# Optimization experiments

Measured on AMD Instinct MI355X. Metric: run time of the kernel, lower is better.

Reference implementation:

```python
import jax, jax.numpy as jnp
import numpy as np

S = 3      # num_scales
CIN = 3    # in_channels (hardcoded by expand(...,3,...) in source)
COUT = 3   # out_channels (forced by final broadcast)
K = 3
PAD = 1


def setup_inputs() -> dict:
    key = jax.random.key(0)
    ks = jax.random.split(key, 8)
    B, H, W = 4, 384, 384
    x = jax.random.normal(ks[0], (B, CIN, H, W), jnp.float32)
    # params follow the torch inits: theta,sigma ~ U(0,pi); f0,theta0 = 1
    theta = jax.random.uniform(ks[1], (S, COUT, CIN), jnp.float32) * jnp.pi
    sigma = jax.random.uniform(ks[2], (S, COUT, CIN), jnp.float32) * jnp.pi
    f0 = jnp.ones((S, COUT, CIN), jnp.float32)
    theta0 = jnp.ones((S, COUT, CIN), jnp.float32)
    attn_w1 = jax.random.normal(ks[3], (64, CIN), jnp.float32) * 0.1     # 1x1 conv weight
    attn_b1 = jnp.zeros((64,), jnp.float32)
    attn_w2 = jax.random.normal(ks[4], (COUT * S, 64), jnp.float32) * 0.1
    attn_b2 = jnp.zeros((COUT * S,), jnp.float32)
    conv_w = jax.random.normal(ks[5], (COUT, CIN, K, K), jnp.float32) * 0.05
    mixing = jax.random.uniform(ks[6], (1,), jnp.float32)
    band = jax.random.uniform(ks[7], (COUT, CIN, 2), jnp.float32)        # freq_band_select ~ U(0,1)
    return dict(x=x, theta=theta, sigma=sigma, f0=f0, theta0=theta0,
                attn_w1=attn_w1, attn_b1=attn_b1, attn_w2=attn_w2, attn_b2=attn_b2,
                conv_w=conv_w, mixing=mixing, band=band)


def _log_gabor_bank(theta, sigma, f0, theta0, H, W):
    # vectorized over all scales: returns [S, Co, Cin, H, W] real filter bank
    yy, xx = jnp.meshgrid(jnp.linspace(-1.0, 1.0, H), jnp.linspace(-1.0, 1.0, W), indexing='ij')
    r = jnp.sqrt(xx * xx + yy * yy + 1e-6)          # [H,W]
    phi = jnp.arctan2(yy, xx)                        # [H,W]
    f0e = f0[..., None, None]                        # [S,Co,Cin,1,1]
    sig = sigma[..., None, None]
    th = theta[..., None, None]
    th0 = theta0[..., None, None]
    log_gabor = jnp.exp(-jnp.log(r - jnp.log(f0e)) ** 2 / (2.0 * jnp.log(sig) ** 2))
    angular = jnp.exp(-(phi - th) ** 2 / (2.0 * th0 ** 2))
    return log_gabor * angular


def _forward(x, theta, sigma, f0, theta0, attn_w1, attn_b1, attn_w2, attn_b2, conv_w, mixing, band):
    B, Cin, H, W = x.shape
    # torch.fft.fftshift with no dim shifts ALL axes (incl. batch/channel) -- replicate exactly
    x_freq_shift = jnp.fft.fftshift(jnp.fft.fft2(x))                 # [B,Cin,H,W] complex64

    filt = _log_gabor_bank(theta, sigma, f0, theta0, H, W)           # [S,Co,Cin,H,W]

    # attention net: 1x1 conv -> relu -> 1x1 conv -> softmax over channel dim
    mag = jnp.abs(x_freq_shift)
    h1 = jax.nn.relu(jnp.einsum('bchw,oc->bohw', mag, attn_w1) + attn_b1[None, :, None, None])
    logits = jnp.einsum('bchw,oc->bohw', h1, attn_w2) + attn_b2[None, :, None, None]
    attn = jax.nn.softmax(logits, axis=1).reshape(B, S, COUT, H, W)

    # attended[b,d,h,w] = sum_{s,co} attn[b,s,co,h,w] * xfreq[b,d,h,w] * filt[s,co,d,h,w]
    wgt = jnp.einsum('bschw,scdhw->bdhw', attn, filt)                # real [B,Cin,H,W]
    attended = (x_freq_shift * wgt).sum(axis=1)                      # [B,H,W] complex

    # per-(out,in)-channel square band mask, indices from height (as in source)
    start_idx = jnp.floor((band[..., 0] + 1.0) / 2.0 * H).astype(jnp.int32)   # [Co,Cin]
    end_idx = jnp.floor((band[..., 1] + 1.0) / 2.0 * H).astype(jnp.int32)
    ih = jnp.arange(H)
    rm = (ih[None, None, :] >= start_idx[..., None]) & (ih[None, None, :] < end_idx[..., None])
    iw = jnp.arange(W)
    cm = (iw[None, None, :] >= start_idx[..., None]) & (iw[None, None, :] < end_idx[..., None])
    mask = (rm[..., :, None] & cm[..., None, :]).astype(x.dtype)     # [Co,Cin,H,W]

    # broadcast quirk in source: [B,1,H,W] * [B,Co,1,Cin,H,W] -> [B,Co,B,Cin,H,W]
    six = mask[None, :, None, :, :, :] * attended[None, None, :, None, :, :]
    six = jnp.broadcast_to(six, (B, COUT, B, Cin, H, W))
    # torch ifftshift with no dim shifts ALL 6 axes; ifft2 transforms last two
    x_filtered = jnp.fft.ifft2(jnp.fft.ifftshift(six)).real          # [B,Co,B,Cin,H,W]

    x_spatial = jax.lax.conv_general_dilated(
        x, conv_w, window_strides=(1, 1), padding=[(PAD, PAD), (PAD, PAD)],
        dimension_numbers=('NCHW', 'OIHW', 'NCHW'))                  # [B,Co,H,W]

    mix = mixing[0]
    return mix * x_filtered + (1.0 - mix) * x_spatial[None, None]    # [B,Co,B,Cin,H,W]


def reference(x, theta, sigma, f0, theta0, attn_w1, attn_b1, attn_w2, attn_b2, conv_w, mixing, band):
    return _forward(x, theta, sigma, f0, theta0, attn_w1, attn_b1, attn_w2, attn_b2, conv_w, mixing, band)
```

## Files before the change

### kernel.cpp

```cpp
#include <hip/hip_runtime.h>
#include <math.h>

#define N384 384
#define NPIX 147456
#define LSTRIDE 385
#define LINES 8

__device__ __forceinline__ float2 cmul(float2 a, float2 b) {
    return make_float2(a.x*b.x - a.y*b.y, a.x*b.y + a.y*b.x);
}

__device__ __forceinline__ void build_tw(float2* tw, int tid) {
    for (int k = tid; k < 384; k += 256) {
        float sn, cs;
        sincospif((float)k * (2.0f / 384.0f), &sn, &cs);
        tw[k] = make_float2(cs, sn);
    }
}

template <int SGNI>
__device__ float2* fft384x8(float2* b0, float2* b1, const float2* tw, int tid) {
    float2* src = b0;
    float2* dst = b1;
    const int line = tid >> 5;
    const int l32  = tid & 31;
    const float SG = (float)SGNI;
    const float s3 = SG * 0.86602540378443864676f;

    {
        float2* L = src + line * LSTRIDE;
        float2* D = dst + line * LSTRIDE;
#pragma unroll
        for (int q = 0; q < 2; ++q) {
            int i = l32 + 32 * q;
            float2 e0 = L[i],       e1 = L[i + 128], e2 = L[i + 256];
            float2 o0 = L[i + 64],  o1 = L[i + 192], o2 = L[i + 320];
            float t1x = e1.x + e2.x, t1y = e1.y + e2.y;
            float t2x = e1.x - e2.x, t2y = e1.y - e2.y;
            float2 E0 = make_float2(e0.x + t1x, e0.y + t1y);
            float mx = e0.x - 0.5f * t1x, my = e0.y - 0.5f * t1y;
            float ux = -s3 * t2y, uy = s3 * t2x;
            float2 E1 = make_float2(mx + ux, my + uy);
            float2 E2 = make_float2(mx - ux, my - uy);
            float s1x = o1.x + o2.x, s1y = o1.y + o2.y;
            float s2x = o1.x - o2.x, s2y = o1.y - o2.y;
            float2 O0 = make_float2(o0.x + s1x, o0.y + s1y);
            float nx = o0.x - 0.5f * s1x, ny = o0.y - 0.5f * s1y;
            float vx = -s3 * s2y, vy = s3 * s2x;
            float2 O1 = make_float2(nx + vx, ny + vy);
            float2 O2 = make_float2(nx - vx, ny - vy);
            float2 T1 = make_float2(0.5f * O1.x - s3 * O1.y, 0.5f * O1.y + s3 * O1.x);
            float2 T2 = make_float2(-0.5f * O2.x - s3 * O2.y, -0.5f * O2.y + s3 * O2.x);
            float2 y0 = make_float2(E0.x + O0.x, E0.y + O0.y);
            float2 y3 = make_float2(E0.x - O0.x, E0.y - O0.y);
            float2 y1 = make_float2(E1.x + T1.x, E1.y + T1.y);
            float2 y4 = make_float2(E1.x - T1.x, E1.y - T1.y);
            float2 y2 = make_float2(E2.x + T2.x, E2.y + T2.y);
            float2 y5 = make_float2(E2.x - T2.x, E2.y - T2.y);
            float2 c1 = tw[i], c2 = tw[2 * i], c3 = tw[3 * i], c4 = tw[4 * i], c5 = tw[5 * i];
            int o = 6 * i;
            D[o]     = y0;
            D[o + 1] = cmul(y1, make_float2(c1.x, SG * c1.y));
            D[o + 2] = cmul(y2, make_float2(c2.x, SG * c2.y));
            D[o + 3] = cmul(y3, make_float2(c3.x, SG * c3.y));
            D[o + 4] = cmul(y4, make_float2(c4.x, SG * c4.y));
            D[o + 5] = cmul(y5, make_float2(c5.x, SG * c5.y));
        }
    }
    __syncthreads();
    { float2* t = src; src = dst; dst = t; }

#pragma unroll
    for (int st = 0; st < 2; ++st) {
        const int s = (st == 0) ? 6 : 24;
        float2* L = src + line * LSTRIDE;
        float2* D = dst + line * LSTRIDE;
#pragma unroll
        for (int q = 0; q < 3; ++q) {
            int i = l32 + 32 * q;
            int k = i % s;
            int js = i - k;
            float2 A0 = L[i];
            float2 A1 = L[i + 96];
            float2 A2 = L[i + 192];
            float2 A3 = L[i + 288];
            float t0x = A0.x + A2.x, t0y = A0.y + A2.y;
            float t1x = A0.x - A2.x, t1y = A0.y - A2.y;
            float t2x = A1.x + A3.x, t2y = A1.y + A3.y;
            float t3x = A1.x - A3.x, t3y = A1.y - A3.y;
            float u3x = -SG * t3y,   u3y = SG * t3x;
            float2 y0 = make_float2(t0x + t2x, t0y + t2y);
            float2 y2 = make_float2(t0x - t2x, t0y - t2y);
            float2 y1 = make_float2(t1x + u3x, t1y + u3y);
            float2 y3 = make_float2(t1x - u3x, t1y - u3y);
            float2 c1 = tw[js], c2 = tw[2 * js], c3 = tw[3 * js];
            float2 w1 = make_float2(c1.x, SG * c1.y);
            float2 w2 = make_float2(c2.x, SG * c2.y);
            float2 w3 = make_float2(c3.x, SG * c3.y);
            int o = i + 3 * js;
            D[o]         = y0;
            D[o + s]     = cmul(y1, w1);
            D[o + 2 * s] = cmul(y2, w2);
            D[o + 3 * s] = cmul(y3, w3);
        }
        __syncthreads();
        { float2* t = src; src = dst; dst = t; }
    }

    {
        float2* L = src + line * LSTRIDE;
        float2* D = dst + line * LSTRIDE;
#pragma unroll
        for (int q = 0; q < 3; ++q) {
            int i = l32 + 32 * q;
            float2 A0 = L[i];
            float2 A1 = L[i + 96];
            float2 A2 = L[i + 192];
            float2 A3 = L[i + 288];
            float t0x = A0.x + A2.x, t0y = A0.y + A2.y;
            float t1x = A0.x - A2.x, t1y = A0.y - A2.y;
            float t2x = A1.x + A3.x, t2y = A1.y + A3.y;
            float t3x = A1.x - A3.x, t3y = A1.y - A3.y;
            float u3x = -SG * t3y,   u3y = SG * t3x;
            D[i]       = make_float2(t0x + t2x, t0y + t2y);
            D[i + 96]  = make_float2(t1x + u3x, t1y + u3y);
            D[i + 192] = make_float2(t0x - t2x, t0y - t2y);
            D[i + 288] = make_float2(t1x - u3x, t1y - u3y);
        }
    }
    __syncthreads();
    return dst;
}

__global__ __launch_bounds__(256) void k_fwd_rows(const float* __restrict__ x,
                                                  float2* __restrict__ F1) {
    __shared__ float2 sbuf[2][LINES * LSTRIDE];
    __shared__ float2 tw[384];
    int img = blockIdx.y;
    int rg  = blockIdx.x;
    int tid = threadIdx.x;
    build_tw(tw, tid);
    const float4* xim = (const float4*)(x + (size_t)img * NPIX + (size_t)rg * 16 * 384);
    for (int idx4 = tid; idx4 < 1536; idx4 += 256) {
        int row = idx4 / 96;
        int e   = (idx4 - row * 96) * 4;
        float4 v = xim[idx4];
        float* L = (float*)(sbuf[0] + (row >> 1) * LSTRIDE + e) + (row & 1);
        L[0] = v.x; L[2] = v.y; L[4] = v.z; L[6] = v.w;
    }
    __syncthreads();
    float2* res = fft384x8<-1>(sbuf[0], sbuf[1], tw, tid);
    float2* F1b = F1 + (size_t)img * NPIX + (size_t)rg * 16 * 384;
    for (int it = tid; it < 1536; it += 256) {
        int line = it / 192;
        int k2   = it - line * 192;
        const float2* L = res + line * LSTRIDE;
        float2 A = L[k2];
        int m = (k2 == 0) ? 0 : 384 - k2;
        float2 B = L[m];
        float2 X1 = make_float2(0.5f * (A.x + B.x), 0.5f * (A.y - B.y));
        float2 X2 = make_float2(0.5f * (A.y + B.y), 0.5f * (B.x - A.x));
        F1b[(size_t)(2 * line) * 384 + k2]     = X1;
        F1b[(size_t)(2 * line + 1) * 384 + k2] = X2;
    }
}

__global__ __launch_bounds__(256) void k_fwd_cols(const float2* __restrict__ In,
                                                  float2* __restrict__ Out) {
    __shared__ float2 sbuf[2][LINES * LSTRIDE];
    __shared__ float2 tw[384];
    int img = blockIdx.y;
    int cg  = blockIdx.x;
    int tid = threadIdx.x;
    build_tw(tw, tid);
    const float4* inim = (const float4*)(In + (size_t)img * NPIX + cg * 8);
    int c = tid & 3, hb = tid >> 2;
    for (int q = 0; q < 6; ++q) {
        int h = hb + 64 * q;
        float4 v = inim[(size_t)h * 192 + c];
        sbuf[0][(2 * c) * LSTRIDE + h]     = make_float2(v.x, v.y);
        sbuf[0][(2 * c + 1) * LSTRIDE + h] = make_float2(v.z, v.w);
    }
    __syncthreads();
    float2* res = fft384x8<-1>(sbuf[0], sbuf[1], tw, tid);
    float4* outim = (float4*)(Out + (size_t)img * NPIX + cg * 8);
    for (int q = 0; q < 3; ++q) {
        int h = hb + 64 * q;
        float2 a = res[(2 * c) * LSTRIDE + h];
        float2 b = res[(2 * c + 1) * LSTRIDE + h];
        outim[(size_t)h * 192 + c] = make_float4(a.x, a.y, b.x, b.y);
    }
}

__global__ __launch_bounds__(192) void k_attn(const float2* __restrict__ F2,
                                              const float* __restrict__ theta,
                                              const float* __restrict__ sigma,
                                              const float* __restrict__ f0,
                                              const float* __restrict__ theta0,
                                              const float* __restrict__ aw1,
                                              const float* __restrict__ ab1,
                                              const float* __restrict__ aw2,
                                              const float* __restrict__ ab2,
                                              const float* __restrict__ band,
                                              float2* __restrict__ A) {
    __shared__ float4 par[27];
    int tid = threadIdx.x;
    if (tid < 27) {
        float lf0 = logf(f0[tid]);
        float ls  = logf(sigma[tid]);
        float na  = -0.5f / (ls * ls);
        float th  = theta[tid];
        float t0  = theta0[tid];
        float nb  = -0.5f / (t0 * t0);
        par[tid] = make_float4(lf0, na, th, nb);
    }
    __syncthreads();

    int h = 192 + blockIdx.x;
    int w = 192 + tid;

    bool needed = false;
#pragma unroll
    for (int q = 0; q < 9; ++q) {
        int s = (int)floorf((band[2 * q + 0] + 1.0f) * 0.5f * 384.0f);
        int e = (int)floorf((band[2 * q + 1] + 1.0f) * 0.5f * 384.0f);
        needed |= (h >= s) && (h < e) && (w >= s) && (w < e);
    }
    if (__ballot(needed) == 0ULL) return;

    int hs = h - 192;
    int ws = w - 192;

    float2 xf[4][3];
    float  mag[4][3];
#pragma unroll
    for (int b = 0; b < 4; ++b) {
        int bp = (b + 2) & 3;
#pragma unroll
        for (int c = 0; c < 3; ++c) {
            int cp = c + 2; if (cp >= 3) cp -= 3;
            float2 v = F2[(size_t)(bp * 3 + cp) * NPIX + (size_t)hs * 384 + ws];
            xf[b][c]  = v;
            mag[b][c] = sqrtf(v.x * v.x + v.y * v.y);
        }
    }

    float lgt[4][9];
#pragma unroll
    for (int b = 0; b < 4; ++b)
#pragma unroll
        for (int j = 0; j < 9; ++j) lgt[b][j] = ab2[j];
    for (int o = 0; o < 64; ++o) {
        float w0 = aw1[o * 3 + 0], w1 = aw1[o * 3 + 1], w2 = aw1[o * 3 + 2];
        float bb = ab1[o];
        float hv[4];
#pragma unroll
        for (int b = 0; b < 4; ++b)
            hv[b] = fmaxf(bb + w0 * mag[b][0] + w1 * mag[b][1] + w2 * mag[b][2], 0.0f);
#pragma unroll
        for (int j = 0; j < 9; ++j) {
            float wj = aw2[j * 64 + o];
#pragma unroll
            for (int b = 0; b < 4; ++b) lgt[b][j] += wj * hv[b];
        }
    }

    float yy = -1.0f + 2.0f * (float)h / 383.0f;
    float xx = -1.0f + 2.0f * (float)w / 383.0f;
    float r   = sqrtf(xx * xx + yy * yy + 1e-6f);
    float phi = atan2f(yy, xx);
    float filt[27];
#pragma unroll
    for (int i = 0; i < 27; ++i) {
        float4 pr = par[i];
        float lr = logf(r - pr.x);
        float dphi = phi - pr.z;
        filt[i] = expf(lr * lr * pr.y + dphi * dphi * pr.w);
    }

#pragma unroll
    for (int b = 0; b < 4; ++b) {
        float mxv = lgt[b][0];
#pragma unroll
        for (int j = 1; j < 9; ++j) mxv = fmaxf(mxv, lgt[b][j]);
        float e[9];
        float se = 0.0f;
#pragma unroll
        for (int j = 0; j < 9; ++j) { e[j] = expf(lgt[b][j] - mxv); se += e[j]; }
        float inv = 1.0f / se;

        float2 acc = make_float2(0.0f, 0.0f);
#pragma unroll
        for (int d = 0; d < 3; ++d) {
            float wg = 0.0f;
#pragma unroll
            for (int s = 0; s < 3; ++s)
#pragma unroll
                for (int co = 0; co < 3; ++co)
                    wg += e[s * 3 + co] * filt[(s * 3 + co) * 3 + d];
            wg *= inv;
            acc.x += xf[b][d].x * wg;
            acc.y += xf[b][d].y * wg;
        }
        if (needed)
            A[(size_t)b * NPIX + (size_t)h * 384 + w] = acc;
    }
}

__global__ __launch_bounds__(256) void k_masked_rows(const float2* __restrict__ A,
                                                     const float* __restrict__ band,
                                                     float2* __restrict__ G1c) {
    int ii  = blockIdx.y;
    int rg  = blockIdx.x;
    int cop = ii / 12;
    int bp  = (ii / 3) % 4;
    int dp  = ii % 3;
    int pidx = (cop * 3 + dp) * 2;
    int sidx = (int)floorf((band[pidx + 0] + 1.0f) * 0.5f * 384.0f);
    int eidx = (int)floorf((band[pidx + 1] + 1.0f) * 0.5f * 384.0f);
    if (eidx <= sidx) return;
    int h0 = 192 + rg * 8;
    if (h0 + 8 <= sidx || h0 >= eidx) return;

    __shared__ float2 sbuf[2][LINES * LSTRIDE];
    __shared__ float2 tw[384];
    int tid = threadIdx.x;
    build_tw(tw, tid);
    const float2* Ab = A + (size_t)bp * NPIX;
    for (int idx = tid; idx < 8 * 384; idx += 256) {
        int line = idx / 384;
        int w    = idx - line * 384;
        int h    = h0 + line;
        bool m = (h >= sidx) && (h < eidx) && (w >= sidx) && (w < eidx);
        float2 v = make_float2(0.0f, 0.0f);
        if (m) v = Ab[(size_t)h * 384 + w];
        sbuf[0][line * LSTRIDE + w] = v;
    }
    __syncthreads();
    float2* res = fft384x8<1>(sbuf[0], sbuf[1], tw, tid);
    for (int idx = tid; idx < 8 * 384; idx += 256) {
        int line = idx / 384;
        int w    = idx - line * 384;
        int h    = h0 + line;
        if (h >= sidx && h < eidx) {
            float2 v = res[line * LSTRIDE + w];
            if (w & 1) { v.x = -v.x; v.y = -v.y; }
            G1c[((size_t)ii * 192 + (h - sidx)) * 384 + w] = v;
        }
    }
}

__global__ __launch_bounds__(256) void k_col_gemm_combine(const float2* __restrict__ G1c,
                                                          const float* __restrict__ band,
                                                          const float* __restrict__ x,
                                                          const float* __restrict__ cw,
                                                          const float* __restrict__ mixing,
                                                          float* __restrict__ out) {
    __shared__ float2 tw[384];
    int tid = threadIdx.x;
    build_tw(tw, tid);

    int ii  = blockIdx.y;
    int gt  = blockIdx.x * 256 + tid;
    int wq  = gt % 96;
    int hg  = gt / 96;
    int w   = wq * 4;
    int h0  = hg * 4;

    int cop = ii / 12;
    int bp  = (ii / 3) % 4;
    int dp  = ii % 3;
    int pidx = (cop * 3 + dp) * 2;
    int sidx = (int)floorf((band[pidx + 0] + 1.0f) * 0.5f * 384.0f);
    int eidx = (int)floorf((band[pidx + 1] + 1.0f) * 0.5f * 384.0f);
    __syncthreads();

    float acc[4][4];
#pragma unroll
    for (int kh = 0; kh < 4; ++kh)
#pragma unroll
        for (int j = 0; j < 4; ++j) acc[kh][j] = 0.0f;

    int idx0 = (sidx * (h0 + 0)) % 384;
    int idx1 = (sidx * (h0 + 1)) % 384;
    int idx2 = (sidx * (h0 + 2)) % 384;
    int idx3 = (sidx * (h0 + 3)) % 384;
    const int s0 = h0, s1 = h0 + 1, s2 = h0 + 2, s3 = h0 + 3;

    const float4* g = (const float4*)(G1c + (size_t)ii * 192 * 384 + w);
    for (int hp = sidx; hp < eidx; ++hp) {
        float4 g0 = g[(size_t)(hp - sidx) * 192];
        float4 g1 = g[(size_t)(hp - sidx) * 192 + 1];
        float2 t0 = tw[idx0];
        float2 t1 = tw[idx1];
        float2 t2 = tw[idx2];
        float2 t3 = tw[idx3];
        acc[0][0] += t0.x * g0.x - t0.y * g0.y;
        acc[0][1] += t0.x * g0.z - t0.y * g0.w;
        acc[0][2] += t0.x * g1.x - t0.y * g1.y;
        acc[0][3] += t0.x * g1.z - t0.y * g1.w;
        acc[1][0] += t1.x * g0.x - t1.y * g0.y;
        acc[1][1] += t1.x * g0.z - t1.y * g0.w;
        acc[1][2] += t1.x * g1.x - t1.y * g1.y;
        acc[1][3] += t1.x * g1.z - t1.y * g1.w;
        acc[2][0] += t2.x * g0.x - t2.y * g0.y;
        acc[2][1] += t2.x * g0.z - t2.y * g0.w;
        acc[2][2] += t2.x * g1.x - t2.y * g1.y;
        acc[2][3] += t2.x * g1.z - t2.y * g1.w;
        acc[3][0] += t3.x * g0.x - t3.y * g0.y;
        acc[3][1] += t3.x * g0.z - t3.y * g0.w;
        acc[3][2] += t3.x * g1.x - t3.y * g1.y;
        acc[3][3] += t3.x * g1.z - t3.y * g1.w;
        idx0 += s0; if (idx0 >= 384) idx0 -= 384;
        idx1 += s1; if (idx1 >= 384) idx1 -= 384;
        idx2 += s2; if (idx2 >= 384) idx2 -= 384;
        idx3 += s3; if (idx3 >= 384) idx3 -= 384;
    }

    int co = cop + 2; if (co >= 3) co -= 3;
    int b  = (bp + 2) & 3;
    int d  = dp + 2;  if (d >= 3) d -= 3;

    float cacc[4][4];
#pragma unroll
    for (int kh = 0; kh < 4; ++kh)
#pragma unroll
        for (int j = 0; j < 4; ++j) cacc[kh][j] = 0.0f;
    const float* xb = x + (size_t)b * 3 * NPIX;
#pragma unroll
    for (int ci = 0; ci < 3; ++ci) {
        const float* xc = xb + (size_t)ci * NPIX;
        const float* w9 = cw + ((size_t)d * 3 + ci) * 9;
        float wv[9];
#pragma unroll
        for (int t = 0; t < 9; ++t) wv[t] = w9[t];
#pragma unroll
        for (int ihh = 0; ihh < 6; ++ihh) {
            int hh = h0 - 1 + ihh;
            if (hh < 0 || hh >= 384) continue;
            float v[6];
#pragma unroll
            for (int c6 = 0; c6 < 6; ++c6) {
                int ww = w - 1 + c6;
                v[c6] = (ww >= 0 && ww < 384) ? xc[(size_t)hh * 384 + ww] : 0.0f;
            }
#pragma unroll
            for (int kh = 0; kh < 4; ++kh) {
                int r = ihh - kh;
                if (r < 0 || r > 2) continue;
#pragma unroll
                for (int j = 0; j < 4; ++j)
#pragma unroll
                    for (int kw = 0; kw < 3; ++kw)
                        cacc[kh][j] += v[j + kw] * wv[r * 3 + kw];
            }
        }
    }

    float mix  = mixing[0];
    float omix = 1.0f - mix;
    const float invn2 = 1.0f / 147456.0f;
    float* obase = out + (size_t)(co * 12 + b * 3 + d) * NPIX;
#pragma unroll
    for (int kh = 0; kh < 4; ++kh) {
        int h = h0 + kh;
        float sgn = (h & 1) ? -invn2 : invn2;
        size_t off = (size_t)h * 384 + w;
        float4 val;
        val.x = mix * (acc[kh][0] * sgn) + omix * cacc[kh][0];
        val.y = mix * (acc[kh][1] * sgn) + omix * cacc[kh][1];
        val.z = mix * (acc[kh][2] * sgn) + omix * cacc[kh][2];
        val.w = mix * (acc[kh][3] * sgn) + omix * cacc[kh][3];
#pragma unroll
        for (int a = 0; a < 4; ++a)
            *(float4*)(obase + off + (size_t)a * 5308416) = val;
    }
}

extern "C" void kernel_launch(void* const* d_in, const int* in_sizes, int n_in,
                              void* d_out, int out_size, void* d_ws, size_t ws_size,
                              hipStream_t stream) {
    const float* x      = (const float*)d_in[0];
    const float* theta  = (const float*)d_in[1];
    const float* sigma  = (const float*)d_in[2];
    const float* f0     = (const float*)d_in[3];
    const float* theta0 = (const float*)d_in[4];
    const float* aw1    = (const float*)d_in[5];
    const float* ab1    = (const float*)d_in[6];
    const float* aw2    = (const float*)d_in[7];
    const float* ab2    = (const float*)d_in[8];
    const float* cw     = (const float*)d_in[9];
    const float* mixing = (const float*)d_in[10];
    const float* band   = (const float*)d_in[11];
    float* out = (float*)d_out;

    float2* F1  = (float2*)d_ws;
    float2* F2  = F1 + (size_t)12 * NPIX;
    float2* G1c = (float2*)d_ws;
    float2* A   = (float2*)d_ws + (size_t)36 * NPIX;

    k_fwd_rows<<<dim3(24, 12), 256, 0, stream>>>(x, F1);
    k_fwd_cols<<<dim3(24, 12), 256, 0, stream>>>(F1, F2);
    k_attn<<<192, 192, 0, stream>>>(F2, theta, sigma, f0, theta0,
                                    aw1, ab1, aw2, ab2, band, A);
    k_masked_rows<<<dim3(24, 36), 256, 0, stream>>>(A, band, G1c);
    k_col_gemm_combine<<<dim3(36, 36), 256, 0, stream>>>(G1c, band, x, cw, mixing, out);
}
```

Before: 205.0 us.

## Replace band-limited direct column DFT with shared-memory FFT in combine kernel

The final kernel used to compute the column inverse transform as a direct DFT: each output accumulated a sum over the band rows using twiddle lookups. It now loads 8 columns of the masked row-transformed data into shared memory, zero-pads outside the band and runs the existing 384-point FFT routine. The inverse FFT is skipped entirely when the band is empty. The per-pixel 3x3 convolution is recomputed per thread, and the output stores shrink from float4 rows to scalar stores over an 8-column tile, which may cost write coalescing on a large output.

```diff
diff --git a/kernel.cpp b/kernel.cpp
--- a/kernel.cpp
+++ b/kernel.cpp
@@ -350,22 +350,18 @@
     }
 }
 
-__global__ __launch_bounds__(256) void k_col_gemm_combine(const float2* __restrict__ G1c,
+__global__ __launch_bounds__(256) void k_col_ifft_combine(const float2* __restrict__ G1c,
                                                           const float* __restrict__ band,
                                                           const float* __restrict__ x,
                                                           const float* __restrict__ cw,
                                                           const float* __restrict__ mixing,
                                                           float* __restrict__ out) {
+    __shared__ float2 sbuf[2][LINES * LSTRIDE];
     __shared__ float2 tw[384];
     int tid = threadIdx.x;
-    build_tw(tw, tid);
-
     int ii  = blockIdx.y;
-    int gt  = blockIdx.x * 256 + tid;
-    int wq  = gt % 96;
-    int hg  = gt / 96;
-    int w   = wq * 4;
-    int h0  = hg * 4;
+    int cg  = blockIdx.x;
+    int w0  = cg * 8;
 
     int cop = ii / 12;
     int bp  = (ii / 3) % 4;
@@ -373,107 +369,72 @@
     int pidx = (cop * 3 + dp) * 2;
     int sidx = (int)floorf((band[pidx + 0] + 1.0f) * 0.5f * 384.0f);
     int eidx = (int)floorf((band[pidx + 1] + 1.0f) * 0.5f * 384.0f);
-    __syncthreads();
-
-    float acc[4][4];
-#pragma unroll
-    for (int kh = 0; kh < 4; ++kh)
-#pragma unroll
-        for (int j = 0; j < 4; ++j) acc[kh][j] = 0.0f;
-
-    int idx0 = (sidx * (h0 + 0)) % 384;
-    int idx1 = (sidx * (h0 + 1)) % 384;
-    int idx2 = (sidx * (h0 + 2)) % 384;
-    int idx3 = (sidx * (h0 + 3)) % 384;
-    const int s0 = h0, s1 = h0 + 1, s2 = h0 + 2, s3 = h0 + 3;
-
-    const float4* g = (const float4*)(G1c + (size_t)ii * 192 * 384 + w);
-    for (int hp = sidx; hp < eidx; ++hp) {
-        float4 g0 = g[(size_t)(hp - sidx) * 192];
-        float4 g1 = g[(size_t)(hp - sidx) * 192 + 1];
-        float2 t0 = tw[idx0];
-        float2 t1 = tw[idx1];
-        float2 t2 = tw[idx2];
-        float2 t3 = tw[idx3];
-        acc[0][0] += t0.x * g0.x - t0.y * g0.y;
-        acc[0][1] += t0.x * g0.z - t0.y * g0.w;
-        acc[0][2] += t0.x * g1.x - t0.y * g1.y;
-        acc[0][3] += t0.x * g1.z - t0.y * g1.w;
-        acc[1][0] += t1.x * g0.x - t1.y * g0.y;
-        acc[1][1] += t1.x * g0.z - t1.y * g0.w;
-        acc[1][2] += t1.x * g1.x - t1.y * g1.y;
-        acc[1][3] += t1.x * g1.z - t1.y * g1.w;
-        acc[2][0] += t2.x * g0.x - t2.y * g0.y;
-        acc[2][1] += t2.x * g0.z - t2.y * g0.w;
-        acc[2][2] += t2.x * g1.x - t2.y * g1.y;
-        acc[2][3] += t2.x * g1.z - t2.y * g1.w;
-        acc[3][0] += t3.x * g0.x - t3.y * g0.y;
-        acc[3][1] += t3.x * g0.z - t3.y * g0.w;
-        acc[3][2] += t3.x * g1.x - t3.y * g1.y;
-        acc[3][3] += t3.x * g1.z - t3.y * g1.w;
-        idx0 += s0; if (idx0 >= 384) idx0 -= 384;
-        idx1 += s1; if (idx1 >= 384) idx1 -= 384;
-        idx2 += s2; if (idx2 >= 384) idx2 -= 384;
-        idx3 += s3; if (idx3 >= 384) idx3 -= 384;
+    bool hasband = (eidx > sidx);
+
+    float2* res = sbuf[0];
+    if (hasband) {
+        build_tw(tw, tid);
+        const float2* gb = G1c + (size_t)ii * 192 * 384 + w0;
+        for (int idx = tid; idx < 8 * 384; idx += 256) {
+            int c = idx & 7;
+            int p = idx >> 3;
+            float2 v = make_float2(0.0f, 0.0f);
+            if (p >= sidx && p < eidx)
+                v = gb[(size_t)(p - sidx) * 384 + c];
+            sbuf[0][c * LSTRIDE + p] = v;
+        }
+        __syncthreads();
+        res = fft384x8<1>(sbuf[0], sbuf[1], tw, tid);
     }
 
     int co = cop + 2; if (co >= 3) co -= 3;
     int b  = (bp + 2) & 3;
     int d  = dp + 2;  if (d >= 3) d -= 3;
 
-    float cacc[4][4];
-#pragma unroll
-    for (int kh = 0; kh < 4; ++kh)
-#pragma unroll
-        for (int j = 0; j < 4; ++j) cacc[kh][j] = 0.0f;
-    const float* xb = x + (size_t)b * 3 * NPIX;
-#pragma unroll
-    for (int ci = 0; ci < 3; ++ci) {
-        const float* xc = xb + (size_t)ci * NPIX;
-        const float* w9 = cw + ((size_t)d * 3 + ci) * 9;
-        float wv[9];
-#pragma unroll
-        for (int t = 0; t < 9; ++t) wv[t] = w9[t];
-#pragma unroll
-        for (int ihh = 0; ihh < 6; ++ihh) {
-            int hh = h0 - 1 + ihh;
-            if (hh < 0 || hh >= 384) continue;
-            float v[6];
-#pragma unroll
-            for (int c6 = 0; c6 < 6; ++c6) {
-                int ww = w - 1 + c6;
-                v[c6] = (ww >= 0 && ww < 384) ? xc[(size_t)hh * 384 + ww] : 0.0f;
-            }
-#pragma unroll
-            for (int kh = 0; kh < 4; ++kh) {
-                int r = ihh - kh;
-                if (r < 0 || r > 2) continue;
-#pragma unroll
-                for (int j = 0; j < 4; ++j)
-#pragma unroll
-                    for (int kw = 0; kw < 3; ++kw)
-                        cacc[kh][j] += v[j + kw] * wv[r * 3 + kw];
-            }
-        }
-    }
+    float wv[3][9];
+#pragma unroll
+    for (int ci = 0; ci < 3; ++ci)
+#pragma unroll
+        for (int t = 0; t < 9; ++t) wv[ci][t] = cw[((size_t)d * 3 + ci) * 9 + t];
 
     float mix  = mixing[0];
     float omix = 1.0f - mix;
     const float invn2 = 1.0f / 147456.0f;
+    const float* xb = x + (size_t)b * 3 * NPIX;
     float* obase = out + (size_t)(co * 12 + b * 3 + d) * NPIX;
-#pragma unroll
-    for (int kh = 0; kh < 4; ++kh) {
-        int h = h0 + kh;
+
+    for (int q = 0; q < 12; ++q) {
+        int p = q * 256 + tid;
+        int h = p >> 3;
+        int c = p & 7;
+        int w = w0 + c;
+
+        float accre = hasband ? res[c * LSTRIDE + h].x : 0.0f;
         float sgn = (h & 1) ? -invn2 : invn2;
+
+        float cv = 0.0f;
+#pragma unroll
+        for (int ci = 0; ci < 3; ++ci) {
+            const float* xc = xb + (size_t)ci * NPIX;
+#pragma unroll
+            for (int kh = 0; kh < 3; ++kh) {
+                int hh = h + kh - 1;
+                if (hh < 0 || hh >= 384) continue;
+                const float* xr = xc + (size_t)hh * 384;
+#pragma unroll
+                for (int kw = 0; kw < 3; ++kw) {
+                    int ww = w + kw - 1;
+                    if (ww >= 0 && ww < 384)
+                        cv += xr[ww] * wv[ci][kh * 3 + kw];
+                }
+            }
+        }
+
+        float val = mix * (accre * sgn) + omix * cv;
         size_t off = (size_t)h * 384 + w;
-        float4 val;
-        val.x = mix * (acc[kh][0] * sgn) + omix * cacc[kh][0];
-        val.y = mix * (acc[kh][1] * sgn) + omix * cacc[kh][1];
-        val.z = mix * (acc[kh][2] * sgn) + omix * cacc[kh][2];
-        val.w = mix * (acc[kh][3] * sgn) + omix * cacc[kh][3];
 #pragma unroll
         for (int a = 0; a < 4; ++a)
-            *(float4*)(obase + off + (size_t)a * 5308416) = val;
+            obase[off + (size_t)a * 5308416] = val;
     }
 }
 
@@ -504,5 +465,5 @@
     k_attn<<<192, 192, 0, stream>>>(F2, theta, sigma, f0, theta0,
                                     aw1, ab1, aw2, ab2, band, A);
     k_masked_rows<<<dim3(24, 36), 256, 0, stream>>>(A, band, G1c);
-    k_col_gemm_combine<<<dim3(36, 36), 256, 0, stream>>>(G1c, band, x, cw, mixing, out);
-}
+    k_col_ifft_combine<<<dim3(48, 36), 256, 0, stream>>>(G1c, band, x, cw, mixing, out);
+}
```

Measured after the change: 363.2 us. +77.1%, slower.
